# Kernel tuning notes

Hardware: AMD Instinct MI355X
Metric: run time of the kernel (lower is better)

## Reference

```python
import jax, jax.numpy as jnp
import numpy as np

N = 50000      # nodes
E = 400000     # edges
D = 512        # embed_dim
L = 3          # num gcn layers
INNER = (L + 1) * D
EPS = 1e-5     # BatchNorm1d eps


def setup_inputs() -> dict:
    key = jax.random.key(0)
    ks = jax.random.split(key, 6)
    x = jax.random.normal(ks[0], (N, D), dtype=jnp.float32)
    edge_index = jax.random.randint(ks[1], (2, E), 0, N, dtype=jnp.int64)
    Ws = jax.random.normal(ks[2], (L, D, D), dtype=jnp.float32) / np.float32(np.sqrt(D))
    bs = jnp.zeros((L, D), jnp.float32)
    bn_gamma = jnp.ones((INNER,), jnp.float32)
    bn_beta = jnp.zeros((INNER,), jnp.float32)
    out_W = jax.random.normal(ks[3], (INNER, D), dtype=jnp.float32) / np.float32(np.sqrt(INNER))
    out_b = jnp.zeros((D,), jnp.float32)
    return {"x": x, "edge_index": edge_index, "Ws": Ws, "bs": bs,
            "bn_gamma": bn_gamma, "bn_beta": bn_beta, "out_W": out_W, "out_b": out_b}


def _gcn_conv(x, W, b, src, dst):
    # PyG GCNConv: add self-loops, sym-normalize, aggregate source->target.
    h = x @ W                                            # [N, D]
    deg = jnp.zeros((N,), x.dtype).at[dst].add(1.0) + 1.0  # in-degree + self-loop
    dinv = jax.lax.rsqrt(deg)
    norm = dinv[src] * dinv[dst]                         # [E]
    agg = jnp.zeros_like(h).at[dst].add(h[src] * norm[:, None])
    agg = agg + h * (dinv * dinv)[:, None]               # self-loop messages
    return agg + b


def reference(x, edge_index, Ws, bs, bn_gamma, bn_beta, out_W, out_b):
    src, dst = edge_index[0], edge_index[1]
    h = x
    x_cat = [x]
    for l in range(L):                                   # fixed small layer loop
        h = jax.nn.gelu(_gcn_conv(h, Ws[l], bs[l], src, dst), approximate=False)
        x_cat.append(h)
    xc = jnp.concatenate(x_cat, axis=-1)                 # [N, (L+1)*D]
    # BatchNorm1d, training-mode batch statistics (biased variance)
    mean = jnp.mean(xc, axis=0)
    var = jnp.var(xc, axis=0)
    xn = (xc - mean) * jax.lax.rsqrt(var + EPS) * bn_gamma + bn_beta
    return xn @ out_W + out_b                            # [N, D]
```

## Files before the change

### kernel.cpp

```cpp
#include <hip/hip_runtime.h>
#include <math.h>

#define N_NODES 50000
#define N_EDGES 400000
#define DIM 512
#define NLAYER 3
#define INNER 2048
#define BN_EPS 1e-5f
#define MPAD 50176

typedef unsigned short u16;
typedef unsigned int u32;

typedef __attribute__((ext_vector_type(8))) short bf16x8;
typedef __attribute__((ext_vector_type(4))) float f32x4;

__device__ __forceinline__ u16 f2bf(float f) {
  union { float f; u32 u; } v; v.f = f;
  u32 u = v.u;
  u32 r = (u + 0x7FFFu + ((u >> 16) & 1u)) >> 16;
  return (u16)r;
}
__device__ __forceinline__ float bf2f(u16 h) {
  union { u32 u; float f; } v; v.u = ((u32)h) << 16; return v.f;
}

#define GLOAD_LDS16(g, l)                                                       \
  __builtin_amdgcn_global_load_lds(                                             \
      (const __attribute__((address_space(1))) u32*)(g),                        \
      (__attribute__((address_space(3))) u32*)(l), 16, 0, 0)


__global__ void k_deg(const int* __restrict__ ei, int* __restrict__ deg) {
  int e = blockIdx.x * blockDim.x + threadIdx.x;
  if (e < N_EDGES) atomicAdd(&deg[ei[N_EDGES + e]], 1);
}

__global__ void k_dinv(const int* __restrict__ deg, float* __restrict__ dinv) {
  int i = blockIdx.x * blockDim.x + threadIdx.x;
  if (i < N_NODES) dinv[i] = rsqrtf((float)(deg[i] + 1));
}

__global__ __launch_bounds__(1024) void k_scan1(const int* __restrict__ deg,
                                                int* __restrict__ bsum, int n) {
  __shared__ int wsum[16];
  int tid = threadIdx.x;
  int lane = tid & 63, wv = tid >> 6;
  int i = blockIdx.x * 1024 + tid;
  int x = (i < n) ? deg[i] : 0;
#pragma unroll
  for (int d = 1; d < 64; d <<= 1) x += __shfl_xor(x, d, 64);
  if (lane == 0) wsum[wv] = x;
  __syncthreads();
  if (tid == 0) {
    int s = 0;
#pragma unroll
    for (int k = 0; k < 16; k++) s += wsum[k];
    bsum[blockIdx.x] = s;
  }
}

__global__ void k_scan2(int* __restrict__ bsum, int* __restrict__ offs, int nb) {
  int lane = threadIdx.x;
  int v = (lane < nb) ? bsum[lane] : 0;
  int x = v;
#pragma unroll
  for (int d = 1; d < 64; d <<= 1) {
    int y = __shfl_up(x, d, 64);
    if (lane >= d) x += y;
  }
  if (lane < nb) bsum[lane] = x - v;
  if (lane == nb - 1) offs[N_NODES] = x;
}

__global__ __launch_bounds__(1024) void k_scan3(const int* __restrict__ deg,
                                                const int* __restrict__ bsum,
                                                int* __restrict__ offs, int n) {
  __shared__ int wsum[16];
  int tid = threadIdx.x;
  int lane = tid & 63, wv = tid >> 6;
  int i = blockIdx.x * 1024 + tid;
  int v = (i < n) ? deg[i] : 0;
  int x = v;
#pragma unroll
  for (int d = 1; d < 64; d <<= 1) {
    int y = __shfl_up(x, d, 64);
    if (lane >= d) x += y;
  }
  if (lane == 63) wsum[wv] = x;
  __syncthreads();
  if (wv == 0) {
    int w = (lane < 16) ? wsum[lane] : 0;
#pragma unroll
    for (int d = 1; d < 16; d <<= 1) {
      int y = __shfl_up(w, d, 64);
      if (lane >= d) w += y;
    }
    if (lane < 16) wsum[lane] = w;
  }
  __syncthreads();
  if (i < n) offs[i] = bsum[blockIdx.x] + (wv ? wsum[wv - 1] : 0) + x - v;
}

__global__ void k_fill(const int* __restrict__ ei, const int* __restrict__ offs,
                       int* __restrict__ cursor, const float* __restrict__ dinv,
                       int* __restrict__ csr_src, float* __restrict__ csr_norm) {
  int e = blockIdx.x * blockDim.x + threadIdx.x;
  if (e >= N_EDGES) return;
  int s = ei[e];
  int d = ei[N_EDGES + e];
  int p = atomicAdd(&cursor[d], 1);
  int idx = offs[d] + p;
  csr_src[idx] = s;
  csr_norm[idx] = dinv[s] * dinv[d];
}

__global__ void k_convert(const float* __restrict__ src, u16* __restrict__ xcat, int n4) {
  int i = blockIdx.x * blockDim.x + threadIdx.x;
  if (i >= n4) return;
  float4 v = ((const float4*)src)[i];
  uint2 o;
  o.x = (u32)f2bf(v.x) | ((u32)f2bf(v.y) << 16);
  o.y = (u32)f2bf(v.z) | ((u32)f2bf(v.w) << 16);
  int row = i >> 7;
  int c4 = (i & 127) * 4;
  *(uint2*)(xcat + (size_t)row * INNER + c4) = o;
}

__global__ __launch_bounds__(256) void k_transpose_tiled(
    const float* __restrict__ W, const float* __restrict__ scale,
    u16* __restrict__ WT, int K) {
  __shared__ float tile[32][33];
  int k0 = blockIdx.x * 32, j0 = blockIdx.y * 32;
  int c = threadIdx.x & 31, r8 = threadIdx.x >> 5;
#pragma unroll
  for (int rr = 0; rr < 4; rr++) {
    int row = rr * 8 + r8;
    float v = W[(size_t)(k0 + row) * DIM + j0 + c];
    if (scale) v *= scale[k0 + row];
    tile[row][c] = v;
  }
  __syncthreads();
#pragma unroll
  for (int rr = 0; rr < 4; rr++) {
    int row = rr * 8 + r8;
    WT[(size_t)(j0 + row) * K + k0 + c] = f2bf(tile[c][row]);
  }
}

#define BM 256
#define BN 256
#define BK 64

#define STAGE2(t, d)                                                        \
  {                                                                         \
    const u16* a_ = aw + (size_t)(t) * 64;                                  \
    const u16* b_ = bw + (size_t)(t) * 64;                                  \
    u16* al = aL + (d) * 16384;                                             \
    u16* bl = bL + (d) * 16384;                                             \
    GLOAD_LDS16(a_, al);                                                    \
    GLOAD_LDS16(a_ + (size_t)16 * lda, al + 512);                           \
    GLOAD_LDS16(a_ + 32, al + 8192);                                        \
    GLOAD_LDS16(a_ + (size_t)16 * lda + 32, al + 8192 + 512);               \
    GLOAD_LDS16(b_, bl);                                                    \
    GLOAD_LDS16(b_ + (size_t)16 * K, bl + 512);                             \
    GLOAD_LDS16(b_ + 32, bl + 8192);                                        \
    GLOAD_LDS16(b_ + (size_t)16 * K + 32, bl + 8192 + 512);                 \
  }

#define TILE_COMPUTE(d)                                                     \
  {                                                                         \
    const u16* ab = arp + (d) * 16384;                                      \
    const u16* bb = brp + (d) * 16384;                                      \
    bf16x8 af[4][2], bfr[4][2];                                             \
    _Pragma("unroll") for (int ii = 0; ii < 4; ii++)                        \
      _Pragma("unroll") for (int s = 0; s < 2; s++)                         \
        af[ii][s] = *(const bf16x8*)(ab + s * 8192 + ii * 512);             \
    _Pragma("unroll") for (int j = 0; j < 4; j++)                           \
      _Pragma("unroll") for (int s = 0; s < 2; s++)                         \
        bfr[j][s] = *(const bf16x8*)(bb + s * 8192 + j * 512);              \
    __builtin_amdgcn_s_setprio(1);                                          \
    _Pragma("unroll") for (int ii = 0; ii < 4; ii++)                        \
      _Pragma("unroll") for (int j = 0; j < 4; j++)                         \
        _Pragma("unroll") for (int s = 0; s < 2; s++)                       \
          acc[ii][j] = __builtin_amdgcn_mfma_f32_16x16x32_bf16(             \
              af[ii][s], bfr[j][s], acc[ii][j], 0, 0, 0);                   \
    __builtin_amdgcn_s_setprio(0);                                          \
    _Pragma("unroll") for (int ii = 0; ii < 4; ii++)                        \
      _Pragma("unroll") for (int s = 0; s < 2; s++)                         \
        af[ii][s] = *(const bf16x8*)(ab + s * 8192 + (4 + ii) * 512);       \
    __builtin_amdgcn_s_setprio(1);                                          \
    _Pragma("unroll") for (int ii = 0; ii < 4; ii++)                        \
      _Pragma("unroll") for (int j = 0; j < 4; j++)                         \
        _Pragma("unroll") for (int s = 0; s < 2; s++)                       \
          acc[4 + ii][j] = __builtin_amdgcn_mfma_f32_16x16x32_bf16(         \
              af[ii][s], bfr[j][s], acc[4 + ii][j], 0, 0, 0);               \
    __builtin_amdgcn_s_setprio(0);                                          \
  }

__global__ __launch_bounds__(512, 2) void gemm_bt(
    const u16* __restrict__ A, int lda,
    const u16* __restrict__ Bt, const float* __restrict__ bias,
    float* __restrict__ Cf, u16* __restrict__ Cb, int M, int K) {
  __shared__ __align__(16) u16 As_[2 * 2 * 256 * 32];
  __shared__ __align__(16) u16 Bs_[2 * 2 * 256 * 32];
  int tid = threadIdx.x;
  int w = tid >> 6, lane = tid & 63;
  int wr = w >> 2, wc = w & 3;

  int nwg = gridDim.x;
  int flat = blockIdx.x;
  int swz = flat;
  if ((nwg & 7) == 0) swz = (flat & 7) * (nwg >> 3) + (flat >> 3);
  int mb = swz >> 1, nb = swz & 1;
  int m0 = mb * BM, n0 = nb * BN;

  int sr = lane >> 2;
  int sc = (lane & 3) * 8;
  const u16* aw = A + (size_t)(m0 + w * 32 + sr) * lda + sc;
  const u16* bw = Bt + (size_t)(n0 + w * 32 + sr) * K + sc;
  u16* aL = &As_[(size_t)(w * 32) * 32];
  u16* bL = &Bs_[(size_t)(w * 32) * 32];

  int lr16 = lane & 15, lq4 = lane >> 4;
  const u16* arp = &As_[(size_t)(wr * 128 + lr16) * 32 + lq4 * 8];
  const u16* brp = &Bs_[(size_t)(wc * 64 + lr16) * 32 + lq4 * 8];

  f32x4 acc[8][4];
#pragma unroll
  for (int i = 0; i < 8; i++)
#pragma unroll
    for (int j = 0; j < 4; j++) acc[i][j] = (f32x4){0.f, 0.f, 0.f, 0.f};

  STAGE2(0, 0);
  STAGE2(1, 1);

  int NT = K >> 6;
  for (int t = 0; t < NT - 1; ++t) {
    asm volatile("s_waitcnt vmcnt(8)" ::: "memory");
    __builtin_amdgcn_s_barrier();
    TILE_COMPUTE(t & 1);
    __builtin_amdgcn_s_barrier();
    if (t + 2 < NT) STAGE2(t + 2, t & 1);
  }
  asm volatile("s_waitcnt vmcnt(0)" ::: "memory");
  __builtin_amdgcn_s_barrier();
  TILE_COMPUTE((NT - 1) & 1);

#pragma unroll
  for (int i = 0; i < 8; i++) {
    int row_b = m0 + wr * 128 + i * 16 + lq4 * 4;
#pragma unroll
    for (int j = 0; j < 4; j++) {
      int col = n0 + wc * 64 + j * 16 + lr16;
      if (Cf) {
        float bv = bias ? bias[col] : 0.f;
#pragma unroll
        for (int r2 = 0; r2 < 4; r2++) {
          int row = row_b + r2;
          if (row < M) Cf[(size_t)row * DIM + col] = acc[i][j][r2] + bv;
        }
      } else {
#pragma unroll
        for (int r2 = 0; r2 < 4; r2++)
          Cb[(size_t)(row_b + r2) * DIM + col] = f2bf(acc[i][j][r2]);
      }
    }
  }
}

__device__ __forceinline__ void accum8(float* a, uint4 h, float w) {
  a[0] += w * bf2f((u16)(h.x & 0xffffu));
  a[1] += w * bf2f((u16)(h.x >> 16));
  a[2] += w * bf2f((u16)(h.y & 0xffffu));
  a[3] += w * bf2f((u16)(h.y >> 16));
  a[4] += w * bf2f((u16)(h.z & 0xffffu));
  a[5] += w * bf2f((u16)(h.z >> 16));
  a[6] += w * bf2f((u16)(h.w & 0xffffu));
  a[7] += w * bf2f((u16)(h.w >> 16));
}

__global__ __launch_bounds__(256) void k_aggregate(
    const u16* __restrict__ hp, const int* __restrict__ offs,
    const int* __restrict__ csr_src, const float* __restrict__ csr_norm,
    const float* __restrict__ dinv, const float* __restrict__ b,
    u16* __restrict__ out_slice) {
  int v = blockIdx.x * 4 + (threadIdx.x >> 6);
  if (v >= N_NODES) return;
  int lane = threadIdx.x & 63;
  int c8 = lane * 8;
  float acc[8];
#pragma unroll
  for (int i = 0; i < 8; i++) acc[i] = 0.f;

  int e0 = offs[v], e1 = offs[v + 1];
  int e = e0;
  for (; e + 4 <= e1; e += 4) {
    int s0 = csr_src[e], s1 = csr_src[e + 1], s2 = csr_src[e + 2], s3 = csr_src[e + 3];
    float w0 = csr_norm[e], w1 = csr_norm[e + 1], w2 = csr_norm[e + 2], w3 = csr_norm[e + 3];
    uint4 h0 = *(const uint4*)(hp + (size_t)s0 * DIM + c8);
    uint4 h1 = *(const uint4*)(hp + (size_t)s1 * DIM + c8);
    uint4 h2 = *(const uint4*)(hp + (size_t)s2 * DIM + c8);
    uint4 h3 = *(const uint4*)(hp + (size_t)s3 * DIM + c8);
    accum8(acc, h0, w0);
    accum8(acc, h1, w1);
    accum8(acc, h2, w2);
    accum8(acc, h3, w3);
  }
  for (; e < e1; e++) {
    int s = csr_src[e];
    float w = csr_norm[e];
    uint4 hv = *(const uint4*)(hp + (size_t)s * DIM + c8);
    accum8(acc, hv, w);
  }
  float di = dinv[v];
  uint4 hv = *(const uint4*)(hp + (size_t)v * DIM + c8);
  accum8(acc, hv, di * di);
  const float4* bb = (const float4*)(b + c8);
  float4 b0 = bb[0], b1 = bb[1];
  acc[0] += b0.x; acc[1] += b0.y; acc[2] += b0.z; acc[3] += b0.w;
  acc[4] += b1.x; acc[5] += b1.y; acc[6] += b1.z; acc[7] += b1.w;
#pragma unroll
  for (int i = 0; i < 8; i++)
    acc[i] = 0.5f * acc[i] * (1.f + erff(acc[i] * 0.70710678118654752f));
  uint4 o;
  o.x = (u32)f2bf(acc[0]) | ((u32)f2bf(acc[1]) << 16);
  o.y = (u32)f2bf(acc[2]) | ((u32)f2bf(acc[3]) << 16);
  o.z = (u32)f2bf(acc[4]) | ((u32)f2bf(acc[5]) << 16);
  o.w = (u32)f2bf(acc[6]) | ((u32)f2bf(acc[7]) << 16);
  *(uint4*)(out_slice + (size_t)v * INNER + c8) = o;
}

__global__ void k_bn_stats(const u16* __restrict__ xcat,
                           float* __restrict__ sums, float* __restrict__ sumsq,
                           int rows_per) {
  int c = blockIdx.x * 512 + threadIdx.x * 2;
  int r0 = blockIdx.y * rows_per;
  int r1 = min(N_NODES, r0 + rows_per);
  float s0 = 0.f, ss0 = 0.f, s1 = 0.f, ss1 = 0.f;
  for (int r = r0; r < r1; r++) {
    u32 u = *(const u32*)(xcat + (size_t)r * INNER + c);
    float x0 = bf2f((u16)(u & 0xffffu));
    float x1 = bf2f((u16)(u >> 16));
    s0 += x0; ss0 += x0 * x0;
    s1 += x1; ss1 += x1 * x1;
  }
  atomicAdd(&sums[c], s0);
  atomicAdd(&sumsq[c], ss0);
  atomicAdd(&sums[c + 1], s1);
  atomicAdd(&sumsq[c + 1], ss1);
}

__global__ void k_bn_finalize(const float* __restrict__ sums, const float* __restrict__ sumsq,
                              const float* __restrict__ gamma, const float* __restrict__ beta,
                              float* __restrict__ scale, float* __restrict__ shift) {
  int c = blockIdx.x * blockDim.x + threadIdx.x;
  if (c >= INNER) return;
  float mean = sums[c] / (float)N_NODES;
  float var = sumsq[c] / (float)N_NODES - mean * mean;
  float rstd = rsqrtf(var + BN_EPS);
  float sc = gamma[c] * rstd;
  scale[c] = sc;
  shift[c] = beta[c] - mean * sc;
}

__global__ __launch_bounds__(256) void k_fold_bias(
    const float* __restrict__ outW, const float* __restrict__ shift,
    const float* __restrict__ outb, float* __restrict__ biasp) {
  int r0 = blockIdx.x * 64;
  int c = threadIdx.x * 2;
  float s0 = 0.f, s1 = 0.f;
  for (int r = 0; r < 64; r++) {
    int row = r0 + r;
    float sh = shift[row];
    float2 w = *(const float2*)(outW + (size_t)row * DIM + c);
    s0 += sh * w.x;
    s1 += sh * w.y;
  }
  if (blockIdx.x == 0) { s0 += outb[c]; s1 += outb[c + 1]; }
  atomicAdd(&biasp[c], s0);
  atomicAdd(&biasp[c + 1], s1);
}

extern "C" void kernel_launch(void* const* d_in, const int* in_sizes, int n_in,
                              void* d_out, int out_size, void* d_ws, size_t ws_size,
                              hipStream_t stream) {
  (void)in_sizes; (void)n_in; (void)out_size; (void)ws_size;
  const float* x     = (const float*)d_in[0];
  const int*   ei    = (const int*)d_in[1];
  const float* Ws    = (const float*)d_in[2];
  const float* bs    = (const float*)d_in[3];
  const float* gamma = (const float*)d_in[4];
  const float* beta  = (const float*)d_in[5];
  const float* outW  = (const float*)d_in[6];
  const float* outb  = (const float*)d_in[7];
  float* out = (float*)d_out;
  u16*   hp  = (u16*)d_out;

  char* ws = (char*)d_ws;
  size_t off = 0;
  auto alloc = [&](size_t bytes) -> void* {
    void* p = ws + off;
    off = (off + bytes + 255) & ~(size_t)255;
    return p;
  };
  int*   deg    = (int*)alloc(N_NODES * 4);
  int*   cursor = (int*)alloc(N_NODES * 4);
  float* sums   = (float*)alloc(INNER * 4);
  float* sumsq  = (float*)alloc(INNER * 4);
  float* biasp  = (float*)alloc(DIM * 4);
  size_t zero_bytes = off;
  float* dinv     = (float*)alloc(N_NODES * 4);
  int*   offs     = (int*)alloc((N_NODES + 1) * 4);
  int*   bsum     = (int*)alloc(64 * 4);
  int*   csr_src  = (int*)alloc(N_EDGES * 4);
  float* csr_norm = (float*)alloc(N_EDGES * 4);
  u16*   xcat = (u16*)alloc((size_t)MPAD * INNER * 2);
  u16*   WbT  = (u16*)alloc((size_t)DIM * DIM * 2);
  u16*   WpT  = (u16*)alloc((size_t)INNER * DIM * 2);
  float* scale = (float*)alloc(INNER * 4);
  float* shift = (float*)alloc(INNER * 4);

  const int SCAN_BLOCKS = (N_NODES + 1023) / 1024;

  hipMemsetAsync(d_ws, 0, zero_bytes, stream);
  k_deg<<<(N_EDGES + 255) / 256, 256, 0, stream>>>(ei, deg);
  k_dinv<<<(N_NODES + 255) / 256, 256, 0, stream>>>(deg, dinv);
  k_scan1<<<SCAN_BLOCKS, 1024, 0, stream>>>(deg, bsum, N_NODES);
  k_scan2<<<1, 64, 0, stream>>>(bsum, offs, SCAN_BLOCKS);
  k_scan3<<<SCAN_BLOCKS, 1024, 0, stream>>>(deg, bsum, offs, N_NODES);
  k_fill<<<(N_EDGES + 255) / 256, 256, 0, stream>>>(ei, offs, cursor, dinv, csr_src, csr_norm);
  k_convert<<<((N_NODES * DIM / 4) + 255) / 256, 256, 0, stream>>>(x, xcat, N_NODES * DIM / 4);

  dim3 ggrid((MPAD / BM) * (DIM / BN));
  for (int l = 0; l < NLAYER; l++) {
    k_transpose_tiled<<<dim3(DIM / 32, DIM / 32), 256, 0, stream>>>(
        Ws + (size_t)l * DIM * DIM, nullptr, WbT, DIM);
    gemm_bt<<<ggrid, 512, 0, stream>>>(xcat + (size_t)l * DIM, INNER, WbT, nullptr,
                                       nullptr, hp, N_NODES, DIM);
    k_aggregate<<<(N_NODES + 3) / 4, 256, 0, stream>>>(hp, offs, csr_src, csr_norm, dinv,
                                                       bs + (size_t)l * DIM,
                                                       xcat + (size_t)(l + 1) * DIM);
  }
  k_bn_stats<<<dim3(INNER / 512, 125), 256, 0, stream>>>(xcat, sums, sumsq, 400);
  k_bn_finalize<<<INNER / 256, 256, 0, stream>>>(sums, sumsq, gamma, beta, scale, shift);
  k_transpose_tiled<<<dim3(INNER / 32, DIM / 32), 256, 0, stream>>>(outW, scale, WpT, INNER);
  k_fold_bias<<<INNER / 64, 256, 0, stream>>>(outW, shift, outb, biasp);
  gemm_bt<<<ggrid, 512, 0, stream>>>(xcat, INNER, WpT, biasp,
                                     out, nullptr, N_NODES, INNER);
}
```

Measured before the change: 934.0 us.

## Interleave quarter-tile global-to-LDS loads with MFMA phases in bf16 GEMM

Reworks the GEMM main loop from two whole-tile stages separated by barriers into four sub-phases per K-tile. Each phase issues a quarter of the next tile's global-to-LDS loads between fragment reads and MFMA bursts. The LDS tile layout is reorganised into 64-row halves so each staging quarter frees a distinct region. This aims to overlap memory traffic with matrix-core work and cut barrier stalls, at the cost of more barriers and waits per tile. On the last iteration the current tile is reloaded into the spare buffer, which wastes some traffic.

```diff
diff --git a/kernel.cpp b/kernel.cpp
--- a/kernel.cpp
+++ b/kernel.cpp
@@ -152,58 +152,51 @@
 #define BN 256
 #define BK 64
 
-#define STAGE2(t, d)                                                        \
-  {                                                                         \
-    const u16* a_ = aw + (size_t)(t) * 64;                                  \
-    const u16* b_ = bw + (size_t)(t) * 64;                                  \
-    u16* al = aL + (d) * 16384;                                             \
-    u16* bl = bL + (d) * 16384;                                             \
-    GLOAD_LDS16(a_, al);                                                    \
-    GLOAD_LDS16(a_ + (size_t)16 * lda, al + 512);                           \
-    GLOAD_LDS16(a_ + 32, al + 8192);                                        \
-    GLOAD_LDS16(a_ + (size_t)16 * lda + 32, al + 8192 + 512);               \
-    GLOAD_LDS16(b_, bl);                                                    \
-    GLOAD_LDS16(b_ + (size_t)16 * K, bl + 512);                             \
-    GLOAD_LDS16(b_ + 32, bl + 8192);                                        \
-    GLOAD_LDS16(b_ + (size_t)16 * K + 32, bl + 8192 + 512);                 \
-  }
-
-#define TILE_COMPUTE(d)                                                     \
-  {                                                                         \
-    const u16* ab = arp + (d) * 16384;                                      \
-    const u16* bb = brp + (d) * 16384;                                      \
-    bf16x8 af[4][2], bfr[4][2];                                             \
-    _Pragma("unroll") for (int ii = 0; ii < 4; ii++)                        \
-      _Pragma("unroll") for (int s = 0; s < 2; s++)                         \
-        af[ii][s] = *(const bf16x8*)(ab + s * 8192 + ii * 512);             \
-    _Pragma("unroll") for (int j = 0; j < 4; j++)                           \
-      _Pragma("unroll") for (int s = 0; s < 2; s++)                         \
-        bfr[j][s] = *(const bf16x8*)(bb + s * 8192 + j * 512);              \
-    __builtin_amdgcn_s_setprio(1);                                          \
-    _Pragma("unroll") for (int ii = 0; ii < 4; ii++)                        \
-      _Pragma("unroll") for (int j = 0; j < 4; j++)                         \
-        _Pragma("unroll") for (int s = 0; s < 2; s++)                       \
-          acc[ii][j] = __builtin_amdgcn_mfma_f32_16x16x32_bf16(             \
-              af[ii][s], bfr[j][s], acc[ii][j], 0, 0, 0);                   \
-    __builtin_amdgcn_s_setprio(0);                                          \
-    _Pragma("unroll") for (int ii = 0; ii < 4; ii++)                        \
-      _Pragma("unroll") for (int s = 0; s < 2; s++)                         \
-        af[ii][s] = *(const bf16x8*)(ab + s * 8192 + (4 + ii) * 512);       \
-    __builtin_amdgcn_s_setprio(1);                                          \
-    _Pragma("unroll") for (int ii = 0; ii < 4; ii++)                        \
-      _Pragma("unroll") for (int j = 0; j < 4; j++)                         \
-        _Pragma("unroll") for (int s = 0; s < 2; s++)                       \
-          acc[4 + ii][j] = __builtin_amdgcn_mfma_f32_16x16x32_bf16(         \
-              af[ii][s], bfr[j][s], acc[4 + ii][j], 0, 0, 0);               \
-    __builtin_amdgcn_s_setprio(0);                                          \
-  }
+#define STAGE_A(MH, TS, SD)                                                  \
+  GLOAD_LDS16(a_base + (size_t)((MH) * 64) * lda + (TS) * 64,                \
+              aL + (SD) * 16384 + (MH) * 8192);                              \
+  GLOAD_LDS16(a_base + (size_t)((MH) * 64 + 128) * lda + (TS) * 64,          \
+              aL + (SD) * 16384 + (MH) * 8192 + 4096);
+
+#define STAGE_B(NH, TS, SD)                                                  \
+  GLOAD_LDS16(b_base + (size_t)((NH) * 32) * K + (TS) * 64,                  \
+              bL + (SD) * 16384 + (NH) * 8192);                              \
+  GLOAD_LDS16(b_base + (size_t)((NH) * 32 + 128) * K + (TS) * 64,            \
+              bL + (SD) * 16384 + (NH) * 8192 + 4096);
+
+#define FRAG_A(D, MH)                                                        \
+  _Pragma("unroll") for (int fi = 0; fi < 4; fi++)                           \
+    _Pragma("unroll") for (int s = 0; s < 2; s++)                            \
+      af[fi][s] = *(const bf16x8*)(arp + (D) * 16384 + (MH) * 8192 +         \
+                                   s * 2048 + fi * 512);
+
+#define FRAG_B(D, NH, BF)                                                    \
+  _Pragma("unroll") for (int fj = 0; fj < 2; fj++)                           \
+    _Pragma("unroll") for (int s = 0; s < 2; s++)                            \
+      BF[fj][s] = *(const bf16x8*)(brp + (D) * 16384 + (NH) * 8192 +         \
+                                   s * 2048 + fj * 512);
+
+#define MFMA16(AI, BF, BJ)                                                   \
+  __builtin_amdgcn_s_setprio(1);                                             \
+  _Pragma("unroll") for (int fi = 0; fi < 4; fi++)                           \
+    _Pragma("unroll") for (int fj = 0; fj < 2; fj++)                         \
+      _Pragma("unroll") for (int s = 0; s < 2; s++)                          \
+        acc[(AI) + fi][(BJ) + fj] = __builtin_amdgcn_mfma_f32_16x16x32_bf16( \
+            af[fi][s], BF[fj][s], acc[(AI) + fi][(BJ) + fj], 0, 0, 0);       \
+  __builtin_amdgcn_s_setprio(0);
+
+#define WAIT_VM4 asm volatile("s_waitcnt vmcnt(4)" ::: "memory")
+#define BAR asm volatile("s_barrier" ::: "memory")
+#define LGKM0                                                                \
+  asm volatile("s_waitcnt lgkmcnt(0)" ::: "memory");                         \
+  __builtin_amdgcn_sched_barrier(0)
 
 __global__ __launch_bounds__(512, 2) void gemm_bt(
     const u16* __restrict__ A, int lda,
     const u16* __restrict__ Bt, const float* __restrict__ bias,
     float* __restrict__ Cf, u16* __restrict__ Cb, int M, int K) {
-  __shared__ __align__(16) u16 As_[2 * 2 * 256 * 32];
-  __shared__ __align__(16) u16 Bs_[2 * 2 * 256 * 32];
+  __shared__ __align__(16) u16 As_[2 * 16384];
+  __shared__ __align__(16) u16 Bs_[2 * 16384];
   int tid = threadIdx.x;
   int w = tid >> 6, lane = tid & 63;
   int wr = w >> 2, wc = w & 3;
@@ -215,16 +208,17 @@
   int mb = swz >> 1, nb = swz & 1;
   int m0 = mb * BM, n0 = nb * BN;
 
-  int sr = lane >> 2;
-  int sc = (lane & 3) * 8;
-  const u16* aw = A + (size_t)(m0 + w * 32 + sr) * lda + sc;
-  const u16* bw = Bt + (size_t)(n0 + w * 32 + sr) * K + sc;
-  u16* aL = &As_[(size_t)(w * 32) * 32];
-  u16* bL = &Bs_[(size_t)(w * 32) * 32];
+  int srow = (w & 3) * 16 + (lane >> 2);
+  int scol = (w >> 2) * 32 + (lane & 3) * 8;
+  const u16* a_base = A + (size_t)(m0 + srow) * lda + scol;
+  int brow = ((srow >> 5) * 64) + (srow & 31);
+  const u16* b_base = Bt + (size_t)(n0 + brow) * K + scol;
+  u16* aL = &As_[w * 512];
+  u16* bL = &Bs_[w * 512];
 
   int lr16 = lane & 15, lq4 = lane >> 4;
-  const u16* arp = &As_[(size_t)(wr * 128 + lr16) * 32 + lq4 * 8];
-  const u16* brp = &Bs_[(size_t)(wc * 64 + lr16) * 32 + lq4 * 8];
+  const u16* arp = &As_[wr * 4096 + lr16 * 32 + lq4 * 8];
+  const u16* brp = &Bs_[(wc >> 1) * 4096 + (wc & 1) * 1024 + lr16 * 32 + lq4 * 8];
 
   f32x4 acc[8][4];
 #pragma unroll
@@ -232,20 +226,39 @@
 #pragma unroll
     for (int j = 0; j < 4; j++) acc[i][j] = (f32x4){0.f, 0.f, 0.f, 0.f};
 
-  STAGE2(0, 0);
-  STAGE2(1, 1);
-
+  STAGE_A(0, 0, 0);
+  STAGE_B(0, 0, 0);
+  STAGE_B(1, 0, 0);
+  STAGE_A(1, 0, 0);
+
+  bf16x8 af[4][2], bf0[2][2], bf1[2][2];
   int NT = K >> 6;
-  for (int t = 0; t < NT - 1; ++t) {
-    asm volatile("s_waitcnt vmcnt(8)" ::: "memory");
-    __builtin_amdgcn_s_barrier();
-    TILE_COMPUTE(t & 1);
-    __builtin_amdgcn_s_barrier();
-    if (t + 2 < NT) STAGE2(t + 2, t & 1);
+  for (int t = 0; t < NT; ++t) {
+    int d = t & 1, sd = d ^ 1;
+    int ts = (t + 1 < NT) ? t + 1 : t;
+    WAIT_VM4;
+    BAR;
+    FRAG_A(d, 0);
+    FRAG_B(d, 0, bf0);
+    STAGE_A(0, ts, sd);
+    LGKM0;
+    MFMA16(0, bf0, 0);
+    WAIT_VM4;
+    BAR;
+    FRAG_B(d, 1, bf1);
+    STAGE_B(0, ts, sd);
+    LGKM0;
+    MFMA16(0, bf1, 2);
+    WAIT_VM4;
+    BAR;
+    FRAG_A(d, 1);
+    STAGE_B(1, ts, sd);
+    LGKM0;
+    MFMA16(4, bf0, 0);
+    STAGE_A(1, ts, sd);
+    MFMA16(4, bf1, 2);
   }
   asm volatile("s_waitcnt vmcnt(0)" ::: "memory");
-  __builtin_amdgcn_s_barrier();
-  TILE_COMPUTE((NT - 1) & 1);
 
 #pragma unroll
   for (int i = 0; i < 8; i++) {
```

Measured after the change: 878.3 us. 6.0% less time.
